# Performance work log

Measured on AMD Instinct MI355X. Metric: run time of the kernel, lower is better.

Reference implementation:

```python
import jax, jax.numpy as jnp
import numpy as np
import math

B, A, T = 64, 23, 128          # batch, num_agents, max seq len
D, AE, S, H = 256, 32, 6, 8    # d_model, agent_encoding_dim, static_dim, heads
DK = D // H                     # 32
DM = D + AE                     # 288, MHA q/k/v dim
NEG = -1e10                     # masked_fill constant from source


def sinusoidal_pe(pos, d):
    # pos: int array [...], returns [..., d] standard transformer PE at positions pos
    half = jnp.arange(d // 2, dtype=jnp.float32)
    div = jnp.exp(-half * (math.log(10000.0) * 2.0 / d))          # [d/2]
    ang = pos[..., None].astype(jnp.float32) * div                # [..., d/2]
    return jnp.stack([jnp.sin(ang), jnp.cos(ang)], axis=-1).reshape(*pos.shape, d)


def setup_inputs() -> dict:
    key = jax.random.key(0)
    ks = jax.random.split(key, 20)
    std = 0.02
    data = jax.random.normal(ks[0], (B, A, T), jnp.float32)
    lengths = jax.random.randint(ks[1], (B, A), 0, T + 1).astype(jnp.int32)   # mask arg = lengths
    t = jnp.arange(T, dtype=jnp.int32)
    time = jnp.where(t[None, None, :] < lengths[:, :, None], t[None, None, :], -1)  # [B,A,T], -1 = pad
    static = jax.random.normal(ks[2], (B, S), jnp.float32)
    # per-agent Linear(1, D): weight [A, D], bias [A, D]
    W_embed = std * jax.random.normal(ks[3], (A, D), jnp.float32)
    b_embed = std * jax.random.normal(ks[4], (A, D), jnp.float32)
    E_var = std * jax.random.normal(ks[5], (A, AE), jnp.float32)            # VariateEncoding table
    W_static = std * jax.random.normal(ks[6], (S, D), jnp.float32)
    b_static = jnp.zeros((D,), jnp.float32)
    Wq = std * jax.random.normal(ks[7], (DM, D), jnp.float32); bq = jnp.zeros((D,), jnp.float32)
    Wk = std * jax.random.normal(ks[8], (DM, D), jnp.float32); bk = jnp.zeros((D,), jnp.float32)
    Wv = std * jax.random.normal(ks[9], (DM, D), jnp.float32); bv = jnp.zeros((D,), jnp.float32)
    Wo = std * jax.random.normal(ks[10], (D, DM), jnp.float32); bo = jnp.zeros((DM,), jnp.float32)
    Wg = std * jax.random.normal(ks[11], (DM + D, 1), jnp.float32); bg = jnp.zeros((1,), jnp.float32)
    return dict(data=data, time=time, mask=lengths, static=static,
                W_embed=W_embed, b_embed=b_embed, E_var=E_var,
                W_static=W_static, b_static=b_static,
                Wq=Wq, bq=bq, Wk=Wk, bk=bk, Wv=Wv, bv=bv, Wo=Wo, bo=bo,
                Wg=Wg, bg=bg)


def reference(data, time, mask, static, W_embed, b_embed, E_var, W_static, b_static,
              Wq, bq, Wk, bk, Wv, bv, Wo, bo, Wg, bg):
    lengths = mask                                            # [B,A] sequence lengths
    t = jnp.arange(T)
    valid = t[None, None, :] < lengths[:, :, None]            # [B,A,T] bool
    # mask_matrix[i,:len,:len]=1 double loop -> vectorized outer product
    mask4 = valid[:, :, :, None] & valid[:, :, None, :]       # [B,A,T,T]

    # per-agent Linear(1, D) loop -> batched rank-1 affine, then ReLU
    data_embeds = jax.nn.relu(data[..., None] * W_embed[None, :, None, :]
                              + b_embed[None, :, None, :])    # [B,A,T,D]

    # src_pe: sinusoidal positional encoding at (clamped) time values
    pe = sinusoidal_pe(jnp.maximum(time, 0), D)               # [B,A,T,D]
    src = data_embeds + pe

    # variate (agent-id) embedding concat -> [B,A,T,D+AE]; encoder = identity
    var = jnp.broadcast_to(E_var[None, :, None, :], (B, A, T, AE))
    memory = jnp.concatenate([src, var], axis=-1)             # [B,A,T,DM]

    # time-masked mean pool over T
    time_mask = time >= 0                                     # [B,A,T]
    memory = jnp.where(time_mask[..., None], memory, 0.0)
    counts = time_mask.sum(axis=2).astype(memory.dtype)       # [B,A]
    agentwise = memory.sum(axis=2) / (counts[..., None] + 1e-9)  # [B,A,DM]

    # custom MHA (dim='Time'): q_len = 1 per agent, keys/values over T
    q = jnp.einsum('bae,ed->bad', agentwise, Wq) + bq          # [B,A,D]
    k = jnp.einsum('bate,ed->batd', memory, Wk) + bk           # [B,A,T,D]
    v = jnp.einsum('bate,ed->batd', memory, Wv) + bv
    qh = q.reshape(B, A, H, DK)                                # [B,A,H,DK] (q_len=1 squeezed)
    kh = k.reshape(B, A, T, H, DK).transpose(0, 1, 3, 2, 4)    # [B,A,H,T,DK]
    vh = v.reshape(B, A, T, H, DK).transpose(0, 1, 3, 2, 4)
    scores = jnp.einsum('bahd,bahtd->baht', qh, kh) / math.sqrt(DK)  # [B,A,H,T]
    amask = mask4[:, :, 0, :]                                  # [B,A,T] row 0 of per-agent mask
    scores = jnp.where(amask[:, :, None, :], scores, NEG)
    p = jax.nn.softmax(scores, axis=-1)                        # dropout = eval (identity)
    ctx = jnp.einsum('baht,bahtd->bahd', p, vh).reshape(B, A, D)
    agent_feat = jnp.einsum('bad,de->bae', ctx, Wo) + bo       # [B,A,DM]

    # agent-masked mean pool over agents
    agent_mask = counts > 0                                    # [B,A]
    agent_feat = jnp.where(agent_mask[..., None], agent_feat, 0.0)
    denom = agent_mask.sum(axis=1).astype(agent_feat.dtype) + 1e-9
    aggre = agent_feat.sum(axis=1) / denom[:, None]            # [B,DM]

    static_feat = static @ W_static + b_static                 # [B,D]
    all_feature = jnp.concatenate([aggre, static_feat], axis=-1)  # [B,DM+D]
    return all_feature @ Wg + bg                               # [B,1]


if __name__ == '__main__':
    out = reference(**setup_inputs())
    print(out.shape, jnp.asarray(out).dtype)
```

## Files before the change

kernel.cpp:

```cpp
#include <hip/hip_runtime.h>
#include <math.h>

#define NB 64
#define NA 23
#define NT 128
#define ND 256
#define NAE 32
#define NS 6
#define NH 8
#define NDM 288

#define OFF_PEK    0
#define OFF_PECUM  32768
#define OFF_WKT    65536
#define OFF_VWO    131072
#define OFF_PEMV   133120
#define OFF_EVA    134144
#define OFF_CST    134328
#define OFF_SB     134336
#define OFF_PROBE  134400

__global__ __launch_bounds__(256) void setup1_kernel(
    const float* __restrict__ Wk, const float* __restrict__ Wv,
    const float* __restrict__ Wo, const float* __restrict__ Wg,
    const float* __restrict__ bv, const float* __restrict__ bo,
    const float* __restrict__ W_static, const float* __restrict__ b_static,
    const float* __restrict__ bg, const float* __restrict__ E_var,
    float* __restrict__ ws)
{
    const int blk = blockIdx.x;
    const int tid = threadIdx.x;
    float* PEcum = ws + OFF_PECUM;
    float* WkT   = ws + OFF_WKT;
    float* VWo   = ws + OFF_VWO;
    float* cst   = ws + OFF_CST;

    if (blk < 128) {
        const int g = tid >> 7, t = tid & 127;
        const int e = blk * 2 + g;
        const int i = e >> 1;
        const float kdiv = 0.07195578415606394f;
        const float dv = expf(-(float)i * kdiv);
        const float ang = (float)t * dv;
        const float v = (e & 1) ? cosf(ang) : sinf(ang);
        __shared__ float buf[256];
        buf[tid] = v;
        #pragma unroll
        for (int s = 1; s < 128; s <<= 1) {
            __syncthreads();
            float add = (t >= s) ? buf[tid - s] : 0.f;
            __syncthreads();
            buf[tid] += add;
        }
        __syncthreads();
        PEcum[t * ND + e] = buf[tid];
    } else if (blk < 384) {
        const int j = blk - 128;
        const float scale = 0.17677669529663687f;
        WkT[j * 256 + tid] = Wk[tid * ND + j] * scale;
    } else if (blk < 392) {
        const int h = blk - 384;
        __shared__ float wog[32];
        __shared__ float vext[32];
        __shared__ float vbS;
        {
            const int jj = tid >> 3, sub = tid & 7;
            const int j = h * 32 + jj;
            float acc = 0.f;
            const int m0 = sub * 36;
            #pragma unroll 4
            for (int m = m0; m < m0 + 36; ++m)
                acc = fmaf(Wo[j * NDM + m], Wg[m], acc);
            acc += __shfl_down(acc, 4, 8);
            acc += __shfl_down(acc, 2, 8);
            acc += __shfl_down(acc, 1, 8);
            if (sub == 0) wog[jj] = acc;
        }
        __syncthreads();
        {
            float acc = 0.f;
            #pragma unroll 8
            for (int jj = 0; jj < 32; ++jj)
                acc = fmaf(Wv[tid * ND + h * 32 + jj], wog[jj], acc);
            VWo[h * 256 + tid] = acc;
        }
        if (tid < 32) {
            float acc = 0.f;
            #pragma unroll 8
            for (int jj = 0; jj < 32; ++jj)
                acc = fmaf(Wv[(256 + tid) * ND + h * 32 + jj], wog[jj], acc);
            vext[tid] = acc;
        }
        if (tid == 0) {
            float acc = 0.f;
            #pragma unroll 8
            for (int jj = 0; jj < 32; ++jj)
                acc = fmaf(bv[h * 32 + jj], wog[jj], acc);
            vbS = acc;
        }
        __syncthreads();
        if (tid < NA) {
            float acc = vbS;
            #pragma unroll 8
            for (int ee = 0; ee < 32; ++ee)
                acc = fmaf(E_var[tid * NAE + ee], vext[ee], acc);
            ws[OFF_EVA + tid * NH + h] = acc;
        }
    } else {
        const int i = tid >> 5, sub = tid & 31;
        float acc = 0.f;
        if (i < 6) {
            for (int m = sub; m < 256; m += 32)
                acc = fmaf(W_static[i * ND + m], Wg[NDM + m], acc);
        } else if (i == 6) {
            for (int m = sub; m < 256; m += 32)
                acc = fmaf(b_static[m], Wg[NDM + m], acc);
        } else {
            for (int m = sub; m < NDM; m += 32)
                acc = fmaf(bo[m], Wg[m], acc);
        }
        #pragma unroll
        for (int off = 16; off > 0; off >>= 1)
            acc += __shfl_down(acc, off, 32);
        if (sub == 0) cst[i] = (i == 6) ? acc + bg[0] : acc;
    }
}

__global__ __launch_bounds__(256) void setup2_kernel(
    const float* __restrict__ Wk, float* __restrict__ ws)
{
    const int t = blockIdx.x;
    const int tid = threadIdx.x;
    __shared__ float peS[256];
    {
        const int i = tid >> 1;
        const float kdiv = 0.07195578415606394f;
        const float dv = expf(-(float)i * kdiv);
        const float ang = (float)t * dv;
        peS[tid] = (tid & 1) ? cosf(ang) : sinf(ang);
    }
    __syncthreads();
    {
        float a0 = 0.f, a1 = 0.f, a2 = 0.f, a3 = 0.f;
        #pragma unroll 4
        for (int e = 0; e < 256; e += 4) {
            a0 = fmaf(peS[e],     Wk[ e      * ND + tid], a0);
            a1 = fmaf(peS[e + 1], Wk[(e + 1) * ND + tid], a1);
            a2 = fmaf(peS[e + 2], Wk[(e + 2) * ND + tid], a2);
            a3 = fmaf(peS[e + 3], Wk[(e + 3) * ND + tid], a3);
        }
        const float scale = 0.17677669529663687f;
        ws[OFF_PEK + tid * NT + t] = ((a0 + a1) + (a2 + a3)) * scale;
    }
    {
        const int h = tid >> 5, ee = tid & 31;
        const float* vw = ws + OFF_VWO + h * 256;
        float v = 0.f;
        #pragma unroll
        for (int k = 0; k < 8; ++k)
            v = fmaf(peS[ee + 32 * k], vw[ee + 32 * k], v);
        v += __shfl_down(v, 16, 32);
        v += __shfl_down(v, 8, 32);
        v += __shfl_down(v, 4, 32);
        v += __shfl_down(v, 2, 32);
        v += __shfl_down(v, 1, 32);
        if (ee == 0) ws[OFF_PEMV + h * NT + t] = v;
    }
    if (t == 0 && tid < NB) ws[OFF_SB + tid] = 0.f;
}

#define E_ITER(KCNT) do {                                                    \
    const int e = ebase + ee;                                                \
    const int r = e & 3;                                                     \
    const float2 wb = Wb[half][e];                                           \
    const float4 cq = comboV[e * 4 + (hh ^ r)];                              \
    const float4 cm = comboV[e * 4 + ((2 | hh) ^ r)];                        \
    const float m0 = fmaxf(fmaf(xt0, wb.x, wb.y), 0.f);                      \
    aS[0][0]=fmaf(m0,cq.x,aS[0][0]); aS[0][1]=fmaf(m0,cq.y,aS[0][1]);        \
    aS[0][2]=fmaf(m0,cq.z,aS[0][2]); aS[0][3]=fmaf(m0,cq.w,aS[0][3]);        \
    aM[0][0]=fmaf(m0,cm.x,aM[0][0]); aM[0][1]=fmaf(m0,cm.y,aM[0][1]);        \
    aM[0][2]=fmaf(m0,cm.z,aM[0][2]); aM[0][3]=fmaf(m0,cm.w,aM[0][3]);        \
    const float m1 = fmaxf(fmaf(xt1, wb.x, wb.y), 0.f);                      \
    aS[1][0]=fmaf(m1,cq.x,aS[1][0]); aS[1][1]=fmaf(m1,cq.y,aS[1][1]);        \
    aS[1][2]=fmaf(m1,cq.z,aS[1][2]); aS[1][3]=fmaf(m1,cq.w,aS[1][3]);        \
    aM[1][0]=fmaf(m1,cm.x,aM[1][0]); aM[1][1]=fmaf(m1,cm.y,aM[1][1]);        \
    aM[1][2]=fmaf(m1,cm.z,aM[1][2]); aM[1][3]=fmaf(m1,cm.w,aM[1][3]);        \
    if ((KCNT) == 4) {                                                       \
        const float m2 = fmaxf(fmaf(xt2, wb.x, wb.y), 0.f);                  \
        aS[2][0]=fmaf(m2,cq.x,aS[2][0]); aS[2][1]=fmaf(m2,cq.y,aS[2][1]);    \
        aS[2][2]=fmaf(m2,cq.z,aS[2][2]); aS[2][3]=fmaf(m2,cq.w,aS[2][3]);    \
        aM[2][0]=fmaf(m2,cm.x,aM[2][0]); aM[2][1]=fmaf(m2,cm.y,aM[2][1]);    \
        aM[2][2]=fmaf(m2,cm.z,aM[2][2]); aM[2][3]=fmaf(m2,cm.w,aM[2][3]);    \
        const float m3 = fmaxf(fmaf(xt3, wb.x, wb.y), 0.f);                  \
        aS[3][0]=fmaf(m3,cq.x,aS[3][0]); aS[3][1]=fmaf(m3,cq.y,aS[3][1]);    \
        aS[3][2]=fmaf(m3,cq.z,aS[3][2]); aS[3][3]=fmaf(m3,cq.w,aS[3][3]);    \
        aM[3][0]=fmaf(m3,cm.x,aM[3][0]); aM[3][1]=fmaf(m3,cm.y,aM[3][1]);    \
        aM[3][2]=fmaf(m3,cm.z,aM[3][2]); aM[3][3]=fmaf(m3,cm.w,aM[3][3]);    \
    }                                                                        \
} while (0)

__global__ __launch_bounds__(512) void main_kernel(
    const float* __restrict__ data, const int* __restrict__ lengths,
    const float* __restrict__ W_embed, const float* __restrict__ b_embed,
    const float* __restrict__ E_var,
    const float* __restrict__ Wq, const float* __restrict__ bq,
    float* __restrict__ ws, const int stub)
{
    const int pair = blockIdx.x;
    const int tid  = threadIdx.x;
    const int half = tid >> 8;
    const int lt   = tid & 255;
    const int wgh  = pair * 2 + half;
    const int ah   = wgh % NA;
    const int bh   = wgh / NA;
    const int Lh   = lengths[wgh];

    __shared__ __align__(16) float xs[2][NT];
    __shared__ __align__(16) float ag[2][NDM];
    __shared__ __align__(16) float qs[2][ND];
    __shared__ float2 Wb[2][ND];
    __shared__ __align__(16) float combo[2][ND * 16];
    __shared__ __align__(16) float qkx[2][NH * NT];
    __shared__ float red[2][4];

    const float* PEcum = ws + OFF_PECUM;
    const float* WkT   = ws + OFF_WKT;
    const float* VWo   = ws + OFF_VWO;
    const float* cstp  = ws + OFF_CST;

    if (lt < NT) xs[half][lt] = data[wgh * NT + lt];
    __syncthreads();
    {
        const int e = lt;
        if (Lh > 0) {
            const float We = W_embed[ah * ND + e];
            const float be = b_embed[ah * ND + e];
            Wb[half][e] = make_float2(We, be);
            const float4* x4 = (const float4*)xs[half];
            float s0 = 0.f, s1 = 0.f, s2 = 0.f, s3 = 0.f;
            const int nq = Lh >> 2;
            for (int q = 0; q < nq; ++q) {
                const float4 xv = x4[q];
                s0 += fmaxf(fmaf(xv.x, We, be), 0.f);
                s1 += fmaxf(fmaf(xv.y, We, be), 0.f);
                s2 += fmaxf(fmaf(xv.z, We, be), 0.f);
                s3 += fmaxf(fmaf(xv.w, We, be), 0.f);
            }
            for (int t = nq * 4; t < Lh; ++t)
                s0 += fmaxf(fmaf(xs[half][t], We, be), 0.f);
            ag[half][e] = (((s0 + s1) + (s2 + s3)) + PEcum[(Lh - 1) * ND + e]) / (float)Lh;
        } else {
            Wb[half][e] = make_float2(0.f, 0.f);
            ag[half][e] = 0.f;
        }
    }
    if (lt < NAE) ag[half][ND + lt] = (Lh > 0) ? E_var[ah * NAE + lt] : 0.f;
    __syncthreads();

    {
        const int j = lt;
        const float4* a40 = (const float4*)ag[0];
        const float4* a41 = (const float4*)ag[1];
        const int fi0 = half * 36;
        float c0 = 0.f, c1 = 0.f, c2 = 0.f, c3 = 0.f;
        #pragma unroll 4
        for (int fi = fi0; fi < fi0 + 36; ++fi) {
            const float4 av0 = a40[fi];
            const float4 av1 = a41[fi];
            const int f = fi * 4;
            const float w0 = Wq[ f      * ND + j];
            const float w1 = Wq[(f + 1) * ND + j];
            const float w2 = Wq[(f + 2) * ND + j];
            const float w3 = Wq[(f + 3) * ND + j];
            c0 = fmaf(av0.x, w0, c0); c2 = fmaf(av0.y, w1, c2);
            c0 = fmaf(av0.z, w2, c0); c2 = fmaf(av0.w, w3, c2);
            c1 = fmaf(av1.x, w0, c1); c3 = fmaf(av1.y, w1, c3);
            c1 = fmaf(av1.z, w2, c1); c3 = fmaf(av1.w, w3, c3);
        }
        float* Csc = &combo[0][0];
        Csc[half * 512 +       j] = c0 + c2;
        Csc[half * 512 + 256 + j] = c1 + c3;
    }
    __syncthreads();
    {
        const float* Csc = &combo[0][0];
        qs[half][lt] = bq[lt] + Csc[half * 256 + lt] + Csc[512 + half * 256 + lt];
    }
    __syncthreads();

    {
        const int e = lt;
        const int hb = half;
        const float* wr = WkT + (hb * 128) * 256 + e;
        const float4* q40 = (const float4*)(qs[0] + hb * 128);
        const float4* q41 = (const float4*)(qs[1] + hb * 128);
        float qk0[4], qk1[4];
        #pragma unroll
        for (int h4 = 0; h4 < 4; ++h4) {
            float c00 = 0.f, c01 = 0.f, c10 = 0.f, c11 = 0.f;
            #pragma unroll
            for (int jq = 0; jq < 8; ++jq) {
                const float4 q0 = q40[h4 * 8 + jq];
                const float4 q1 = q41[h4 * 8 + jq];
                const float w0 = wr[(h4 * 32 + jq * 4 + 0) * 256];
                const float w1 = wr[(h4 * 32 + jq * 4 + 1) * 256];
                const float w2 = wr[(h4 * 32 + jq * 4 + 2) * 256];
                const float w3 = wr[(h4 * 32 + jq * 4 + 3) * 256];
                c00 = fmaf(w0, q0.x, c00); c01 = fmaf(w1, q0.y, c01);
                c00 = fmaf(w2, q0.z, c00); c01 = fmaf(w3, q0.w, c01);
                c10 = fmaf(w0, q1.x, c10); c11 = fmaf(w1, q1.y, c11);
                c10 = fmaf(w2, q1.z, c10); c11 = fmaf(w3, q1.w, c11);
            }
            qk0[h4] = c00 + c01;
            qk1[h4] = c10 + c11;
        }
        const int r = e & 3;
        float4* row0 = (float4*)(&combo[0][0]) + e * 4;
        float4* row1 = (float4*)(&combo[1][0]) + e * 4;
        row0[hb ^ r] = make_float4(qk0[0], qk0[1], qk0[2], qk0[3]);
        row1[hb ^ r] = make_float4(qk1[0], qk1[1], qk1[2], qk1[3]);
        const float4 vw = make_float4(VWo[(hb * 4 + 0) * 256 + e],
                                      VWo[(hb * 4 + 1) * 256 + e],
                                      VWo[(hb * 4 + 2) * 256 + e],
                                      VWo[(hb * 4 + 3) * 256 + e]);
        row0[(2 | hb) ^ r] = vw;
        row1[(2 | hb) ^ r] = vw;
    }
    {
        const int h  = tid >> 6;
        const int tq = tid & 63;
        const float* pekt = ws + OFF_PEK;
        const float4* qs40 = (const float4*)(qs[0] + h * 32);
        const float4* qs41 = (const float4*)(qs[1] + h * 32);
        float b00 = 0.f, b01 = 0.f, b10 = 0.f, b11 = 0.f;
        #pragma unroll
        for (int jq = 0; jq < 8; ++jq) {
            const float4 q0 = qs40[jq];
            const float4 q1 = qs41[jq];
            const float* pr = pekt + (h * 32 + jq * 4) * NT + tq;
            const float p00 = pr[0];          const float p01 = pr[64];
            const float p10 = pr[NT];         const float p11 = pr[NT + 64];
            const float p20 = pr[2 * NT];     const float p21 = pr[2 * NT + 64];
            const float p30 = pr[3 * NT];     const float p31 = pr[3 * NT + 64];
            b00 = fmaf(q0.x, p00, b00); b00 = fmaf(q0.y, p10, b00);
            b00 = fmaf(q0.z, p20, b00); b00 = fmaf(q0.w, p30, b00);
            b01 = fmaf(q0.x, p01, b01); b01 = fmaf(q0.y, p11, b01);
            b01 = fmaf(q0.z, p21, b01); b01 = fmaf(q0.w, p31, b01);
            b10 = fmaf(q1.x, p00, b10); b10 = fmaf(q1.y, p10, b10);
            b10 = fmaf(q1.z, p20, b10); b10 = fmaf(q1.w, p30, b10);
            b11 = fmaf(q1.x, p01, b11); b11 = fmaf(q1.y, p11, b11);
            b11 = fmaf(q1.z, p21, b11); b11 = fmaf(q1.w, p31, b11);
        }
        qkx[0][h * NT + tq]      = b00;
        qkx[0][h * NT + tq + 64] = b01;
        qkx[1][h * NT + tq]      = b10;
        qkx[1][h * NT + tq + 64] = b11;
    }
    __syncthreads();

    {
        const int lane = lt & 63;
        const int wv   = lt >> 6;
        const int hh   = wv & 1;
        const int tw   = wv >> 1;
        const int t0   = lane & 15;
        const int c    = lane >> 4;
        const int tb   = tw * 16 + t0;
        const int ebase = c * 64;
        const float4* comboV = (const float4*)(&combo[half][0]);
        float aS[4][4], aM[4][4];
        #pragma unroll
        for (int k = 0; k < 4; ++k)
            #pragma unroll
            for (int j = 0; j < 4; ++j) { aS[k][j] = 0.f; aM[k][j] = 0.f; }
        const float xt0 = xs[half][tb];
        const float xt1 = xs[half][tb + 32];
        const float xt2 = xs[half][tb + 64];
        const float xt3 = xs[half][tb + 96];
        if (!stub && Lh > 64) {
            #pragma unroll 4
            for (int ee = 0; ee < 64; ++ee) E_ITER(4);
        } else if (!stub && Lh > 0) {
            #pragma unroll 4
            for (int ee = 0; ee < 64; ++ee) E_ITER(2);
        }
        #pragma unroll
        for (int k = 0; k < 4; ++k)
            #pragma unroll
            for (int j = 0; j < 4; ++j) {
                float vS = aS[k][j], vM = aM[k][j];
                vS += __shfl_down(vS, 32, 64);
                vS += __shfl_down(vS, 16, 64);
                vM += __shfl_down(vM, 32, 64);
                vM += __shfl_down(vM, 16, 64);
                aS[k][j] = vS; aM[k][j] = vM;
            }
        __syncthreads();
        float* scF = &combo[half][0];
        float* mvF = scF + 1024;
        if (c == 0) {
            #pragma unroll
            for (int k = 0; k < 4; ++k)
                #pragma unroll
                for (int j = 0; j < 4; ++j) {
                    const int h = hh * 4 + j;
                    scF[h * NT + tb + 32 * k] = aS[k][j];
                    mvF[h * NT + tb + 32 * k] = aM[k][j];
                }
        }
    }
    __syncthreads();

    if (Lh > 0) {
        const float* sc   = &combo[half][0];
        const float* mvb  = sc + 1024;
        const float* pemv = ws + OFF_PEMV;
        const int wv = lt >> 6, lane = lt & 63;
        float wsum = 0.f;
        for (int hh2 = 0; hh2 < 2; ++hh2) {
            const int h = wv * 2 + hh2;
            float s1 = (lane < Lh) ? sc[h * NT + lane] + qkx[half][h * NT + lane] : -3e38f;
            float s2 = (lane + 64 < Lh) ? sc[h * NT + 64 + lane] + qkx[half][h * NT + 64 + lane] : -3e38f;
            float mx = fmaxf(s1, s2);
            #pragma unroll
            for (int off = 32; off > 0; off >>= 1)
                mx = fmaxf(mx, __shfl_down(mx, off, 64));
            mx = __shfl(mx, 0, 64);
            const float vbv = ws[OFF_EVA + ah * NH + h];
            float e1 = (lane < Lh) ? __expf(s1 - mx) : 0.f;
            float e2 = (lane + 64 < Lh) ? __expf(s2 - mx) : 0.f;
            float num = e1 * (mvb[h * NT + lane] + pemv[h * NT + lane] + vbv);
            num = fmaf(e2, mvb[h * NT + 64 + lane] + pemv[h * NT + 64 + lane] + vbv, num);
            float den = e1 + e2;
            #pragma unroll
            for (int off = 32; off > 0; off >>= 1) {
                num += __shfl_down(num, off, 64);
                den += __shfl_down(den, off, 64);
            }
            if (lane == 0) wsum += num / den;
        }
        if (lane == 0) red[half][wv] = wsum;
    }
    __syncthreads();
    if (lt == 0 && Lh > 0) {
        float* sbase = ws + (stub ? OFF_PROBE : OFF_SB);
        atomicAdd(sbase + bh,
                  cstp[7] + red[half][0] + red[half][1] + red[half][2] + red[half][3]);
    }
}

__global__ __launch_bounds__(64) void final_kernel(
    const float* __restrict__ statics, const int* __restrict__ lengths,
    const float* __restrict__ ws, float* __restrict__ out)
{
    const int b = threadIdx.x;
    const float* cst = ws + OFF_CST;
    int n = 0;
    for (int a = 0; a < NA; ++a)
        if (lengths[b * NA + a] > 0) ++n;
    float o = ws[OFF_SB + b] / ((float)n + 1e-9f);
    #pragma unroll
    for (int i = 0; i < NS; ++i)
        o = fmaf(statics[b * NS + i], cst[i], o);
    o += cst[6];
    out[b] = o;
}

extern "C" void kernel_launch(void* const* d_in, const int* in_sizes, int n_in,
                              void* d_out, int out_size, void* d_ws, size_t ws_size,
                              hipStream_t stream) {
    const float* data     = (const float*)d_in[0];
    const int*   mask     = (const int*)d_in[2];
    const float* statics  = (const float*)d_in[3];
    const float* W_embed  = (const float*)d_in[4];
    const float* b_embed  = (const float*)d_in[5];
    const float* E_var    = (const float*)d_in[6];
    const float* W_static = (const float*)d_in[7];
    const float* b_static = (const float*)d_in[8];
    const float* Wq       = (const float*)d_in[9];
    const float* bq       = (const float*)d_in[10];
    const float* Wk       = (const float*)d_in[11];
    const float* Wv       = (const float*)d_in[13];
    const float* bv       = (const float*)d_in[14];
    const float* Wo       = (const float*)d_in[15];
    const float* bo       = (const float*)d_in[16];
    const float* Wg       = (const float*)d_in[17];
    const float* bg       = (const float*)d_in[18];
    float* out = (float*)d_out;
    float* ws  = (float*)d_ws;

    setup1_kernel<<<dim3(393), dim3(256), 0, stream>>>(Wk, Wv, Wo, Wg, bv, bo,
                                                       W_static, b_static, bg, E_var, ws);
    setup2_kernel<<<dim3(128), dim3(256), 0, stream>>>(Wk, ws);
    main_kernel<<<dim3(NB * NA / 2), dim3(512), 0, stream>>>(data, mask, W_embed, b_embed,
                                                             E_var, Wq, bq, ws, 0);
    final_kernel<<<dim3(1), dim3(64), 0, stream>>>(statics, mask, ws, out);
    main_kernel<<<dim3(NB * NA / 2), dim3(512), 0, stream>>>(data, mask, W_embed, b_embed,
                                                             E_var, Wq, bq, ws, 1);
}
```

Baseline: 188.1 us.

## Drop stub probe launch, reuse combo LDS for ag/qkx, pad Wb rows

Removes the second stub launch of main_kernel, a leftover timing probe, along with its stub parameter and probe workspace slot. The per-timestep E loop now runs before the qkx computation. That lets the ag and qkx shared arrays live inside the combo buffer, which lowers LDS use per block and could raise occupancy. The Wb array and the combo row swizzle gain a padding offset every 64 entries to reduce LDS bank conflicts. In exchange, the aliasing of combo regions depends on careful barrier ordering, and a misplaced barrier would corrupt values.

```diff
diff --git a/kernel.cpp b/kernel.cpp
--- a/kernel.cpp
+++ b/kernel.cpp
@@ -18,7 +18,6 @@
 #define OFF_EVA    134144
 #define OFF_CST    134328
 #define OFF_SB     134336
-#define OFF_PROBE  134400
 
 __global__ __launch_bounds__(256) void setup1_kernel(
     const float* __restrict__ Wk, const float* __restrict__ Wv,
@@ -171,8 +170,8 @@
 
 #define E_ITER(KCNT) do {                                                    \
     const int e = ebase + ee;                                                \
-    const int r = e & 3;                                                     \
-    const float2 wb = Wb[half][e];                                           \
+    const int r = (e + (e >> 6)) & 3;                                        \
+    const float2 wb = Wb[half][e + (e >> 6)];                                \
     const float4 cq = comboV[e * 4 + (hh ^ r)];                              \
     const float4 cm = comboV[e * 4 + ((2 | hh) ^ r)];                        \
     const float m0 = fmaxf(fmaf(xt0, wb.x, wb.y), 0.f);                      \
@@ -204,7 +203,7 @@
     const float* __restrict__ W_embed, const float* __restrict__ b_embed,
     const float* __restrict__ E_var,
     const float* __restrict__ Wq, const float* __restrict__ bq,
-    float* __restrict__ ws, const int stub)
+    float* __restrict__ ws)
 {
     const int pair = blockIdx.x;
     const int tid  = threadIdx.x;
@@ -216,17 +215,16 @@
     const int Lh   = lengths[wgh];
 
     __shared__ __align__(16) float xs[2][NT];
-    __shared__ __align__(16) float ag[2][NDM];
     __shared__ __align__(16) float qs[2][ND];
-    __shared__ float2 Wb[2][ND];
+    __shared__ float2 Wb[2][ND + 4];
     __shared__ __align__(16) float combo[2][ND * 16];
-    __shared__ __align__(16) float qkx[2][NH * NT];
     __shared__ float red[2][4];
 
     const float* PEcum = ws + OFF_PECUM;
     const float* WkT   = ws + OFF_WKT;
     const float* VWo   = ws + OFF_VWO;
     const float* cstp  = ws + OFF_CST;
+    float* agA = &combo[1][0];
 
     if (lt < NT) xs[half][lt] = data[wgh * NT + lt];
     __syncthreads();
@@ -235,7 +233,7 @@
         if (Lh > 0) {
             const float We = W_embed[ah * ND + e];
             const float be = b_embed[ah * ND + e];
-            Wb[half][e] = make_float2(We, be);
+            Wb[half][e + (e >> 6)] = make_float2(We, be);
             const float4* x4 = (const float4*)xs[half];
             float s0 = 0.f, s1 = 0.f, s2 = 0.f, s3 = 0.f;
             const int nq = Lh >> 2;
@@ -248,19 +246,19 @@
             }
             for (int t = nq * 4; t < Lh; ++t)
                 s0 += fmaxf(fmaf(xs[half][t], We, be), 0.f);
-            ag[half][e] = (((s0 + s1) + (s2 + s3)) + PEcum[(Lh - 1) * ND + e]) / (float)Lh;
+            agA[half * NDM + e] = (((s0 + s1) + (s2 + s3)) + PEcum[(Lh - 1) * ND + e]) / (float)Lh;
         } else {
-            Wb[half][e] = make_float2(0.f, 0.f);
-            ag[half][e] = 0.f;
-        }
-    }
-    if (lt < NAE) ag[half][ND + lt] = (Lh > 0) ? E_var[ah * NAE + lt] : 0.f;
+            Wb[half][e + (e >> 6)] = make_float2(0.f, 0.f);
+            agA[half * NDM + e] = 0.f;
+        }
+    }
+    if (lt < NAE) agA[half * NDM + ND + lt] = (Lh > 0) ? E_var[ah * NAE + lt] : 0.f;
     __syncthreads();
 
     {
         const int j = lt;
-        const float4* a40 = (const float4*)ag[0];
-        const float4* a41 = (const float4*)ag[1];
+        const float4* a40 = (const float4*)(agA);
+        const float4* a41 = (const float4*)(agA + NDM);
         const int fi0 = half * 36;
         float c0 = 0.f, c1 = 0.f, c2 = 0.f, c3 = 0.f;
         #pragma unroll 4
@@ -314,7 +312,7 @@
             qk0[h4] = c00 + c01;
             qk1[h4] = c10 + c11;
         }
-        const int r = e & 3;
+        const int r = (e + (e >> 6)) & 3;
         float4* row0 = (float4*)(&combo[0][0]) + e * 4;
         float4* row1 = (float4*)(&combo[1][0]) + e * 4;
         row0[hb ^ r] = make_float4(qk0[0], qk0[1], qk0[2], qk0[3]);
@@ -326,6 +324,61 @@
         row0[(2 | hb) ^ r] = vw;
         row1[(2 | hb) ^ r] = vw;
     }
+    __syncthreads();
+
+    {
+        const int lane = lt & 63;
+        const int wv   = lt >> 6;
+        const int hh   = wv & 1;
+        const int tw   = wv >> 1;
+        const int t0   = lane & 15;
+        const int c    = lane >> 4;
+        const int tb   = tw * 16 + t0;
+        const int ebase = c * 64;
+        const float4* comboV = (const float4*)(&combo[half][0]);
+        float aS[4][4], aM[4][4];
+        #pragma unroll
+        for (int k = 0; k < 4; ++k)
+            #pragma unroll
+            for (int j = 0; j < 4; ++j) { aS[k][j] = 0.f; aM[k][j] = 0.f; }
+        const float xt0 = xs[half][tb];
+        const float xt1 = xs[half][tb + 32];
+        const float xt2 = xs[half][tb + 64];
+        const float xt3 = xs[half][tb + 96];
+        if (Lh > 64) {
+            #pragma unroll 4
+            for (int ee = 0; ee < 64; ++ee) E_ITER(4);
+        } else if (Lh > 0) {
+            #pragma unroll 4
+            for (int ee = 0; ee < 64; ++ee) E_ITER(2);
+        }
+        #pragma unroll
+        for (int k = 0; k < 4; ++k)
+            #pragma unroll
+            for (int j = 0; j < 4; ++j) {
+                float vS = aS[k][j], vM = aM[k][j];
+                vS += __shfl_down(vS, 32, 64);
+                vS += __shfl_down(vS, 16, 64);
+                vM += __shfl_down(vM, 32, 64);
+                vM += __shfl_down(vM, 16, 64);
+                aS[k][j] = vS; aM[k][j] = vM;
+            }
+        __syncthreads();
+        float* scF = &combo[half][0];
+        float* mvF = scF + 1024;
+        if (c == 0) {
+            #pragma unroll
+            for (int k = 0; k < 4; ++k)
+                #pragma unroll
+                for (int j = 0; j < 4; ++j) {
+                    const int h = hh * 4 + j;
+                    scF[h * NT + tb + 32 * k] = aS[k][j];
+                    mvF[h * NT + tb + 32 * k] = aM[k][j];
+                }
+        }
+    }
+    __syncthreads();
+
     {
         const int h  = tid >> 6;
         const int tq = tid & 63;
@@ -351,76 +404,24 @@
             b11 = fmaf(q1.x, p01, b11); b11 = fmaf(q1.y, p11, b11);
             b11 = fmaf(q1.z, p21, b11); b11 = fmaf(q1.w, p31, b11);
         }
-        qkx[0][h * NT + tq]      = b00;
-        qkx[0][h * NT + tq + 64] = b01;
-        qkx[1][h * NT + tq]      = b10;
-        qkx[1][h * NT + tq + 64] = b11;
-    }
-    __syncthreads();
-
-    {
-        const int lane = lt & 63;
-        const int wv   = lt >> 6;
-        const int hh   = wv & 1;
-        const int tw   = wv >> 1;
-        const int t0   = lane & 15;
-        const int c    = lane >> 4;
-        const int tb   = tw * 16 + t0;
-        const int ebase = c * 64;
-        const float4* comboV = (const float4*)(&combo[half][0]);
-        float aS[4][4], aM[4][4];
-        #pragma unroll
-        for (int k = 0; k < 4; ++k)
-            #pragma unroll
-            for (int j = 0; j < 4; ++j) { aS[k][j] = 0.f; aM[k][j] = 0.f; }
-        const float xt0 = xs[half][tb];
-        const float xt1 = xs[half][tb + 32];
-        const float xt2 = xs[half][tb + 64];
-        const float xt3 = xs[half][tb + 96];
-        if (!stub && Lh > 64) {
-            #pragma unroll 4
-            for (int ee = 0; ee < 64; ++ee) E_ITER(4);
-        } else if (!stub && Lh > 0) {
-            #pragma unroll 4
-            for (int ee = 0; ee < 64; ++ee) E_ITER(2);
-        }
-        #pragma unroll
-        for (int k = 0; k < 4; ++k)
-            #pragma unroll
-            for (int j = 0; j < 4; ++j) {
-                float vS = aS[k][j], vM = aM[k][j];
-                vS += __shfl_down(vS, 32, 64);
-                vS += __shfl_down(vS, 16, 64);
-                vM += __shfl_down(vM, 32, 64);
-                vM += __shfl_down(vM, 16, 64);
-                aS[k][j] = vS; aM[k][j] = vM;
-            }
-        __syncthreads();
-        float* scF = &combo[half][0];
-        float* mvF = scF + 1024;
-        if (c == 0) {
-            #pragma unroll
-            for (int k = 0; k < 4; ++k)
-                #pragma unroll
-                for (int j = 0; j < 4; ++j) {
-                    const int h = hh * 4 + j;
-                    scF[h * NT + tb + 32 * k] = aS[k][j];
-                    mvF[h * NT + tb + 32 * k] = aM[k][j];
-                }
-        }
+        combo[0][2048 + h * NT + tq]      = b00;
+        combo[0][2048 + h * NT + tq + 64] = b01;
+        combo[1][2048 + h * NT + tq]      = b10;
+        combo[1][2048 + h * NT + tq + 64] = b11;
     }
     __syncthreads();
 
     if (Lh > 0) {
         const float* sc   = &combo[half][0];
         const float* mvb  = sc + 1024;
+        const float* qkxp = sc + 2048;
         const float* pemv = ws + OFF_PEMV;
         const int wv = lt >> 6, lane = lt & 63;
         float wsum = 0.f;
         for (int hh2 = 0; hh2 < 2; ++hh2) {
             const int h = wv * 2 + hh2;
-            float s1 = (lane < Lh) ? sc[h * NT + lane] + qkx[half][h * NT + lane] : -3e38f;
-            float s2 = (lane + 64 < Lh) ? sc[h * NT + 64 + lane] + qkx[half][h * NT + 64 + lane] : -3e38f;
+            float s1 = (lane < Lh) ? sc[h * NT + lane] + qkxp[h * NT + lane] : -3e38f;
+            float s2 = (lane + 64 < Lh) ? sc[h * NT + 64 + lane] + qkxp[h * NT + 64 + lane] : -3e38f;
             float mx = fmaxf(s1, s2);
             #pragma unroll
             for (int off = 32; off > 0; off >>= 1)
@@ -442,11 +443,9 @@
         if (lane == 0) red[half][wv] = wsum;
     }
     __syncthreads();
-    if (lt == 0 && Lh > 0) {
-        float* sbase = ws + (stub ? OFF_PROBE : OFF_SB);
-        atomicAdd(sbase + bh,
+    if (lt == 0 && Lh > 0)
+        atomicAdd(ws + OFF_SB + bh,
                   cstp[7] + red[half][0] + red[half][1] + red[half][2] + red[half][3]);
-    }
 }
 
 __global__ __launch_bounds__(64) void final_kernel(
@@ -493,8 +492,6 @@
                                                        W_static, b_static, bg, E_var, ws);
     setup2_kernel<<<dim3(128), dim3(256), 0, stream>>>(Wk, ws);
     main_kernel<<<dim3(NB * NA / 2), dim3(512), 0, stream>>>(data, mask, W_embed, b_embed,
-                                                             E_var, Wq, bq, ws, 0);
+                                                             E_var, Wq, bq, ws);
     final_kernel<<<dim3(1), dim3(64), 0, stream>>>(statics, mask, ws, out);
-    main_kernel<<<dim3(NB * NA / 2), dim3(512), 0, stream>>>(data, mask, W_embed, b_embed,
-                                                             E_var, Wq, bq, ws, 1);
 }
```

After: 151.4 us, median of 2. 1.24x faster.
